# Performance work log

Measured on AMD Instinct MI355X. Metric: run time of the kernel, lower is better.

The kernel has to match this reference:

```python
import jax, jax.numpy as jnp
import numpy as np

# Static config (matches init_kwargs)
N = 1024        # node_num
F = 64          # input_dim (window length)
D = 64          # dim == embed_dim (heads=1)
TOPK = 20
B = 64
EPS = 1e-5      # BatchNorm eps
NEG_SLOPE = 0.2 # GraphLayer leaky_relu slope


def setup_inputs() -> dict:
    key = jax.random.key(0)
    ks = jax.random.split(key, 12)
    s = lambda fan: 1.0 / np.sqrt(fan)
    inp = {
        'data': jax.random.normal(ks[0], (B, N, F), jnp.float32),
        'org_edge_index': jax.random.randint(ks[1], (2, 2048), 0, N),
        'embedding': jax.random.normal(ks[2], (N, D), jnp.float32) * s(D),   # nn.Embedding(node_num, dim), xavier-ish
        'lin_w': jax.random.normal(ks[3], (F, D), jnp.float32) * s(F),       # GraphLayer lin (bias=False)
        'att_i': jax.random.normal(ks[4], (D,), jnp.float32) * s(D),
        'att_j': jax.random.normal(ks[5], (D,), jnp.float32) * s(D),
        'att_em_i': jax.random.normal(ks[6], (D,), jnp.float32) * s(D),
        'att_em_j': jax.random.normal(ks[7], (D,), jnp.float32) * s(D),
        'gnn_bias': jnp.zeros((D,), jnp.float32),
        'bn1_gamma': jnp.ones((D,), jnp.float32),  # GNNLayer.bn
        'bn1_beta': jnp.zeros((D,), jnp.float32),
        'bn2_gamma': jnp.ones((D,), jnp.float32),  # bn_outlayer_in
        'bn2_beta': jnp.zeros((D,), jnp.float32),
        'out_w': jax.random.normal(ks[8], (D, 1), jnp.float32) * s(D),       # OutLayer Linear(dim, 1)
        'out_b': jnp.zeros((1,), jnp.float32),
    }
    return inp


def _batchnorm(x, gamma, beta, axes):
    # training-mode BatchNorm: batch statistics over `axes`, per-feature affine
    mu = jnp.mean(x, axis=axes, keepdims=True)
    var = jnp.var(x, axis=axes, keepdims=True)
    return gamma * (x - mu) * jax.lax.rsqrt(var + EPS) + beta


def reference(data, org_edge_index, embedding, lin_w, att_i, att_j, att_em_i,
              att_em_j, gnn_bias, bn1_gamma, bn1_beta, bn2_gamma, bn2_beta,
              out_w, out_b):
    # --- dynamic graph construction from embedding cosine similarity ---
    w = jax.lax.stop_gradient(embedding)          # weights_arr.detach()
    nrm = jnp.linalg.norm(w, axis=-1)
    cos = (w @ w.T) / jnp.clip(nrm[:, None] * nrm[None, :], 1e-10)
    _, topi = jax.lax.top_k(cos, TOPK)            # [N, TOPK] neighbors j of each target i
    # (torch code drops edges whose cos value is exactly 0 -- measure-zero with
    #  random embeddings; edge count stays N*TOPK. Self edge i->i is always in topk,
    #  matching remove_self_loops + add_self_loops.)

    # --- GraphLayer (GAT-style, heads=1, concat=False, aggr='add') ---
    xl = jnp.einsum('bnf,fd->bnd', data, lin_w)   # linear transform, [B,N,D]
    xj = xl[:, topi]                               # gather neighbor feats [B,N,TOPK,D]
    ej = embedding[topi]                           # neighbor embeddings [N,TOPK,D]
    # alpha = <key_i, att_i||att_em_i> + <key_j, att_j||att_em_j>
    score = (xl @ att_i)[:, :, None] \
          + (embedding @ att_em_i)[None, :, None] \
          + jnp.einsum('bnkd,d->bnk', xj, att_j) \
          + (ej @ att_em_j)[None]                  # [B,N,TOPK]
    alpha = jax.nn.softmax(jax.nn.leaky_relu(score, NEG_SLOPE), axis=-1)
    gnn = jnp.einsum('bnk,bnkd->bnd', alpha, xj) + gnn_bias

    # GNNLayer.bn: BatchNorm1d over B*N samples, D channels
    gnn = _batchnorm(gnn, bn1_gamma, bn1_beta, axes=(0, 1))

    # --- readout ---
    out = gnn * embedding[None]                    # mul with node embedding
    out = jax.nn.relu(_batchnorm(out, bn2_gamma, bn2_beta, axes=(0, 1)))
    # dropout(0.2) -> identity (eval)
    pred = (out @ out_w + out_b).reshape(B, N)     # OutLayer: Linear(D, 1)
    return pred, out
```

## Files before the change

### kernel.cpp

```cpp
#include <hip/hip_runtime.h>

#define NN 1024
#define KK 20
#define BN 65536
#define NEG_SLOPE 0.2f

typedef unsigned short u16;
typedef unsigned int u32;
typedef unsigned long long u64;
typedef __attribute__((ext_vector_type(8))) short bf8;
typedef __attribute__((ext_vector_type(4))) float f32x4;

__device__ __forceinline__ float bf2f(u16 h) {
    return __uint_as_float(((u32)h) << 16);
}
__device__ __forceinline__ u16 f2bf(float f) {
    u32 u = __float_as_uint(f);
    u32 lsb = (u >> 16) & 1u;
    u += 0x7fffu + lsb;
    return (u16)(u >> 16);
}
__device__ __forceinline__ void up2(u32 w, float& a, float& b) {
    a = __uint_as_float(w << 16);
    b = __uint_as_float(w & 0xffff0000u);
}
__device__ __forceinline__ bool is_bf(const void* g1) {
    return *(const u32*)g1 == 0x3F803F80u;
}
template <bool BF>
__device__ __forceinline__ float ldf(const void* p, size_t i) {
    if (BF) return bf2f(((const u16*)p)[i]);
    return ((const float*)p)[i];
}
template <bool BF>
__device__ __forceinline__ void stf(void* p, size_t i, float v) {
    if (BF) ((u16*)p)[i] = f2bf(v);
    else ((float*)p)[i] = v;
}
template <bool BF>
__device__ __forceinline__ void ldf2(const void* p, size_t pairidx, float& a, float& b) {
    if (BF) {
        u32 w = ((const u32*)p)[pairidx];
        up2(w, a, b);
    } else {
        float2 v = ((const float2*)p)[pairidx];
        a = v.x;
        b = v.y;
    }
}

template <bool BF>
__device__ void k1a_body(const void* emb, const void* aei, const void* aej,
                         u16* nwH, u16* nwL, float* e_i, float* e_j, float* stats) {
    __shared__ float sme[4][64], sm2[4][64];
    int tid = threadIdx.x;
    int lane = tid & 63, wave = tid >> 6;
    int n = blockIdx.x * 4 + wave;
    float v = ldf<BF>(emb, n * 64 + lane);
    sme[wave][lane] = v;
    sm2[wave][lane] = v * v;
    float s2 = v * v;
    float si = v * ldf<BF>(aei, lane);
    float sj = v * ldf<BF>(aej, lane);
#pragma unroll
    for (int off = 32; off; off >>= 1) {
        s2 += __shfl_xor(s2, off, 64);
        si += __shfl_xor(si, off, 64);
        sj += __shfl_xor(sj, off, 64);
    }
    float rq = rsqrtf(fmaxf(s2, 1e-20f));
    float x = v * rq;
    u16 h = f2bf(x);
    nwH[n * 64 + lane] = h;
    nwL[n * 64 + lane] = f2bf(x - bf2f(h));
    if (lane == 0) { e_i[n] = si; e_j[n] = sj; }
    __syncthreads();
    if (tid < 64) {
        float u1 = sme[0][tid] + sme[1][tid] + sme[2][tid] + sme[3][tid];
        atomicAdd(&stats[320 + tid], 64.f * u1);
    } else if (tid < 128) {
        int d = tid - 64;
        float u2 = sm2[0][d] + sm2[1][d] + sm2[2][d] + sm2[3][d];
        atomicAdd(&stats[384 + d], 64.f * u2);
    }
}
__global__ __launch_bounds__(256) void k1a_norm(const void* emb, const void* aei, const void* aej,
                                                const void* probe, u16* nwH, u16* nwL,
                                                float* e_i, float* e_j, float* stats) {
    if (is_bf(probe)) k1a_body<true>(emb, aei, aej, nwH, nwL, e_i, e_j, stats);
    else k1a_body<false>(emb, aei, aej, nwH, nwL, e_i, e_j, stats);
}

__global__ __launch_bounds__(256) void k1b_gram(const u16* __restrict__ nwH,
                                                const u16* __restrict__ nwL,
                                                float* __restrict__ G) {
    int tid = threadIdx.x;
    int lane = tid & 63, wave = tid >> 6;
    int c = lane & 15, quad = lane >> 4;
    int rowblk = blockIdx.x >> 4, colblk = blockIdx.x & 15;
    int arow = rowblk * 64 + wave * 16 + c;
    bf8 aH[2], aL[2];
#pragma unroll
    for (int s = 0; s < 2; ++s) {
        aH[s] = *(const bf8*)(nwH + (size_t)arow * 64 + s * 32 + quad * 8);
        aL[s] = *(const bf8*)(nwL + (size_t)arow * 64 + s * 32 + quad * 8);
    }
    f32x4 acc[4] = {{0.f, 0.f, 0.f, 0.f}, {0.f, 0.f, 0.f, 0.f}, {0.f, 0.f, 0.f, 0.f}, {0.f, 0.f, 0.f, 0.f}};
#pragma unroll
    for (int t = 0; t < 4; ++t) {
        int bnode = colblk * 64 + t * 16 + c;
#pragma unroll
        for (int s = 0; s < 2; ++s) {
            bf8 bH = *(const bf8*)(nwH + (size_t)bnode * 64 + s * 32 + quad * 8);
            bf8 bL = *(const bf8*)(nwL + (size_t)bnode * 64 + s * 32 + quad * 8);
            acc[t] = __builtin_amdgcn_mfma_f32_16x16x32_bf16(aH[s], bH, acc[t], 0, 0, 0);
            acc[t] = __builtin_amdgcn_mfma_f32_16x16x32_bf16(aH[s], bL, acc[t], 0, 0, 0);
            acc[t] = __builtin_amdgcn_mfma_f32_16x16x32_bf16(aL[s], bH, acc[t], 0, 0, 0);
        }
    }
#pragma unroll
    for (int t = 0; t < 4; ++t) {
#pragma unroll
        for (int reg = 0; reg < 4; ++reg) {
            int row = rowblk * 64 + wave * 16 + quad * 4 + reg;
            G[(size_t)row * 1024 + colblk * 64 + t * 16 + c] = acc[t][reg];
        }
    }
}

__device__ void k1c_body(int blk, const float* __restrict__ G, int* __restrict__ topi) {
    int lane = threadIdx.x & 63, wave = threadIdx.x >> 6;
    int n = blk * 4 + wave;
    const f32x4* gp = (const f32x4*)(G + (size_t)n * 1024 + lane * 16);
    f32x4 v0 = gp[0], v1 = gp[1], v2 = gp[2], v3 = gp[3];
    float c[16] = {v0.x, v0.y, v0.z, v0.w, v1.x, v1.y, v1.z, v1.w,
                   v2.x, v2.y, v2.z, v2.w, v3.x, v3.y, v3.z, v3.w};
    u32 o[16];
#pragma unroll
    for (int j = 0; j < 16; ++j) {
        u32 u = __float_as_uint(c[j]);
        o[j] = u ^ (u32)(((int)u >> 31) | 0x80000000);
    }
    unsigned mask = 0u;
    int keep = 0;
    for (int r = 0; r < KK; ++r) {
        u32 bo = 0u;
        int bj = 0;
#pragma unroll
        for (int j = 0; j < 16; ++j) {
            bool t = !((mask >> j) & 1u) && o[j] > bo;
            bo = t ? o[j] : bo;
            bj = t ? j : bj;
        }
        u64 key = ((u64)bo << 32) | (u32)(~(u32)(lane * 16 + bj));
#pragma unroll
        for (int off = 32; off; off >>= 1) {
            u64 ok = __shfl_xor((unsigned long long)key, off, 64);
            key = ok > key ? ok : key;
        }
        int bm = (int)((~(u32)key) & 1023u);
        if ((bm >> 4) == lane) mask |= 1u << (bm & 15);
        if (lane == r) keep = bm;
    }
    if (lane < KK) topi[n * KK + lane] = keep;
}

template <bool BF>
__device__ void k2_body(int blk, const void* data, const void* lin_w, const void* att_i,
                        const void* att_j, u16* xl, float* a_i, float* a_j) {
    __shared__ u16 Bl[64 * 72];
    __shared__ u16 Ct[64 * 72];
    int tid = threadIdx.x;
    {
        int k = tid >> 2, n0 = (tid & 3) * 16;
        if (BF) {
            const u16* lw = (const u16*)lin_w;
#pragma unroll
            for (int i = 0; i < 16; ++i) Bl[(n0 + i) * 72 + k] = lw[k * 64 + n0 + i];
        } else {
            const float* lw = (const float*)lin_w;
#pragma unroll
            for (int i = 0; i < 16; ++i) Bl[(n0 + i) * 72 + k] = f2bf(lw[k * 64 + n0 + i]);
        }
    }
    __syncthreads();
    int lane = tid & 63, wave = tid >> 6;
    int c = lane & 15, quad = lane >> 4;
    int m0 = blk * 64 + wave * 16;
    size_t row = (size_t)(m0 + c);
    f32x4 acc[4] = {{0.f, 0.f, 0.f, 0.f}, {0.f, 0.f, 0.f, 0.f}, {0.f, 0.f, 0.f, 0.f}, {0.f, 0.f, 0.f, 0.f}};
#pragma unroll
    for (int s = 0; s < 2; ++s) {
        bf8 a;
        if (BF) {
            a = *(const bf8*)((const u16*)data + row * 64 + s * 32 + quad * 8);
        } else {
            const float* dp = (const float*)data + row * 64 + s * 32 + quad * 8;
            f32x4 x0 = *(const f32x4*)dp;
            f32x4 x1 = *(const f32x4*)(dp + 4);
            a[0] = (short)f2bf(x0.x); a[1] = (short)f2bf(x0.y);
            a[2] = (short)f2bf(x0.z); a[3] = (short)f2bf(x0.w);
            a[4] = (short)f2bf(x1.x); a[5] = (short)f2bf(x1.y);
            a[6] = (short)f2bf(x1.z); a[7] = (short)f2bf(x1.w);
        }
#pragma unroll
        for (int t = 0; t < 4; ++t) {
            bf8 b = *(const bf8*)&Bl[(t * 16 + c) * 72 + s * 32 + quad * 8];
            acc[t] = __builtin_amdgcn_mfma_f32_16x16x32_bf16(a, b, acc[t], 0, 0, 0);
        }
    }
    float wi[4], wj[4];
#pragma unroll
    for (int t = 0; t < 4; ++t) {
        wi[t] = ldf<BF>(att_i, t * 16 + c);
        wj[t] = ldf<BF>(att_j, t * 16 + c);
    }
    float ai4[4] = {0.f, 0.f, 0.f, 0.f}, aj4[4] = {0.f, 0.f, 0.f, 0.f};
#pragma unroll
    for (int t = 0; t < 4; ++t) {
#pragma unroll
        for (int reg = 0; reg < 4; ++reg) {
            float v = acc[t][reg];
            Ct[(wave * 16 + quad * 4 + reg) * 72 + t * 16 + c] = f2bf(v);
            ai4[reg] += v * wi[t];
            aj4[reg] += v * wj[t];
        }
    }
#pragma unroll
    for (int reg = 0; reg < 4; ++reg) {
#pragma unroll
        for (int off = 1; off < 16; off <<= 1) {
            ai4[reg] += __shfl_xor(ai4[reg], off, 64);
            aj4[reg] += __shfl_xor(aj4[reg], off, 64);
        }
    }
    if (c == 0) {
#pragma unroll
        for (int reg = 0; reg < 4; ++reg) {
            a_i[m0 + quad * 4 + reg] = ai4[reg];
            a_j[m0 + quad * 4 + reg] = aj4[reg];
        }
    }
    __syncthreads();
    {
        int r = tid >> 2, seg = tid & 3;
        uint4 v0 = *(const uint4*)&Ct[r * 72 + seg * 16];
        uint4 v1 = *(const uint4*)&Ct[r * 72 + seg * 16 + 8];
        uint4* dst = (uint4*)xl + ((size_t)(blk * 64 + r) * 8 + seg * 2);
        dst[0] = v0;
        dst[1] = v1;
    }
}

__global__ __launch_bounds__(256) void k12_fused(const void* data, const void* lin_w,
                                                 const void* att_i, const void* att_j,
                                                 const void* probe, u16* xl, float* a_i,
                                                 float* a_j, const float* G, int* topi) {
    if (blockIdx.x < 1024) {
        if (is_bf(probe)) k2_body<true>(blockIdx.x, data, lin_w, att_i, att_j, xl, a_i, a_j);
        else k2_body<false>(blockIdx.x, data, lin_w, att_i, att_j, xl, a_i, a_j);
    } else {
        k1c_body(blockIdx.x - 1024, G, topi);
    }
}

template <bool BF>
__device__ void k3_body(const u16* xl, const int* topi, const float* a_i, const float* a_j,
                        const float* e_i, const float* e_j, const void* emb,
                        const void* gnn_bias, void* dout, float* stats) {
    extern __shared__ char smem[];
    u32* slice = (u32*)smem;
    float* aje = (float*)(smem + 131072);
    float* aie = (float*)(smem + 135168);
    uint2* sp = (uint2*)(smem + 136192);
    int tid = threadIdx.x;
    int b = blockIdx.x & 63;
    int q = blockIdx.x >> 6;
    int n0 = q * 256;
    const uint4* src = (const uint4*)(xl + ((size_t)b << 16));
    uint4* dst = (uint4*)slice;
#pragma unroll
    for (int r = 0; r < 8; ++r) dst[r * 1024 + tid] = src[r * 1024 + tid];
    aje[tid] = a_j[(b << 10) + tid] + e_j[tid];
    if (tid < 256) aie[tid] = a_i[(b << 10) + n0 + tid] + e_i[n0 + tid];
    __syncthreads();
    int lane = tid & 63, wave = tid >> 6;
    int half = lane >> 5, hl = lane & 31;
    int hwid = wave * 2 + half;
    float bias0, bias1;
    ldf2<BF>(gnn_bias, hl, bias0, bias1);
    float se[10];
#pragma unroll
    for (int s = 0; s < 10; ++s) se[s] = 0.f;
    int nl0 = hwid * 8;
    u32 tc = 0;
    float al = 0.f;
    {
        int t = (hl < KK) ? topi[(n0 + nl0) * KK + hl] : 0;
        float sc = -3e38f;
        if (hl < KK) {
            sc = aie[nl0] + aje[t];
            sc = sc >= 0.f ? sc : NEG_SLOPE * sc;
        }
        float m = sc;
#pragma unroll
        for (int off = 16; off; off >>= 1) m = fmaxf(m, __shfl_xor(m, off, 32));
        float p = (hl < KK) ? __expf(sc - m) : 0.f;
        float S = p;
#pragma unroll
        for (int off = 16; off; off >>= 1) S += __shfl_xor(S, off, 32);
        tc = (u32)t;
        al = p / S;
    }
    for (int ii = 0; ii < 8; ++ii) {
        int nl = nl0 + ii;
        int n = n0 + nl;
        int pair = (b << 10) + n;
        if (hl < KK) {
            uint2 v; v.x = tc; v.y = __float_as_uint(al);
            sp[hwid * KK + hl] = v;
        }
        u32 tn = 0;
        float aln = 0.f;
        if (ii < 7) {
            int t = (hl < KK) ? topi[(n + 1) * KK + hl] : 0;
            float sc = -3e38f;
            if (hl < KK) {
                sc = aie[nl + 1] + aje[t];
                sc = sc >= 0.f ? sc : NEG_SLOPE * sc;
            }
            float m = sc;
#pragma unroll
            for (int off = 16; off; off >>= 1) m = fmaxf(m, __shfl_xor(m, off, 32));
            float p = (hl < KK) ? __expf(sc - m) : 0.f;
            float S = p;
#pragma unroll
            for (int off = 16; off; off >>= 1) S += __shfl_xor(S, off, 32);
            tn = (u32)t;
            aln = p / S;
        }
        float a0e = 0.f, a0o = 0.f, a1e = 0.f, a1o = 0.f;
#pragma unroll
        for (int k = 0; k < KK; k += 2) {
            uint2 v0 = sp[hwid * KK + k];
            uint2 v1 = sp[hwid * KK + k + 1];
            u32 w0 = slice[(v0.x << 5) + hl];
            u32 w1 = slice[(v1.x << 5) + hl];
            float p0 = __uint_as_float(v0.y);
            float p1 = __uint_as_float(v1.y);
            a0e += p0 * __uint_as_float(w0 << 16);
            a1e += p0 * __uint_as_float(w0 & 0xffff0000u);
            a0o += p1 * __uint_as_float(w1 << 16);
            a1o += p1 * __uint_as_float(w1 & 0xffff0000u);
        }
        float acc0 = a0e + a0o + bias0;
        float acc1 = a1e + a1o + bias1;
        if (BF) {
            u32 pk = (u32)f2bf(acc0) | ((u32)f2bf(acc1) << 16);
            ((u32*)dout)[(BN >> 1) + pair * 32 + hl] = pk;
        } else {
            float2 v2; v2.x = acc0; v2.y = acc1;
            ((float2*)dout)[(BN >> 1) + pair * 32 + hl] = v2;
        }
        float em0, em1;
        ldf2<BF>(emb, n * 32 + hl, em0, em1);
        se[0] += acc0; se[1] += acc1;
        se[2] += acc0 * acc0; se[3] += acc1 * acc1;
        float ge0 = acc0 * em0, ge1 = acc1 * em1;
        se[4] += ge0; se[5] += ge1;
        se[6] += ge0 * ge0; se[7] += ge1 * ge1;
        se[8] += ge0 * em0; se[9] += ge1 * em1;
        tc = tn;
        al = aln;
    }
#pragma unroll
    for (int s = 0; s < 10; ++s) se[s] += __shfl_xor(se[s], 32, 64);
    __syncthreads();
    float* ps = (float*)smem;
    if (half == 0) {
#pragma unroll
        for (int s = 0; s < 5; ++s) {
            ps[wave * 320 + s * 64 + 2 * hl] = se[2 * s];
            ps[wave * 320 + s * 64 + 2 * hl + 1] = se[2 * s + 1];
        }
    }
    __syncthreads();
    if (tid < 320) {
        float s = 0.f;
#pragma unroll
        for (int w = 0; w < 16; ++w) s += ps[w * 320 + tid];
        atomicAdd(&stats[tid], s);
    }
}
__global__ __launch_bounds__(1024) void k3_gnn(const u16* xl, const int* topi, const float* a_i,
                                               const float* a_j, const float* e_i, const float* e_j,
                                               const void* emb, const void* gnn_bias, const void* probe,
                                               void* dout, float* stats) {
    if (is_bf(probe)) k3_body<true>(xl, topi, a_i, a_j, e_i, e_j, emb, gnn_bias, dout, stats);
    else k3_body<false>(xl, topi, a_i, a_j, e_i, e_j, emb, gnn_bias, dout, stats);
}

template <bool BF>
__device__ void k5_body(const void* emb, const float* stats, const void* g1, const void* b1,
                        const void* g2, const void* b2, const void* out_w, const void* out_b,
                        void* dout) {
    int lane = threadIdx.x & 63;
    float P, Q, R;
    {
        int d = lane;
        double inv = 1.0 / 65536.0;
        double S1 = stats[d], S2 = stats[64 + d], T1 = stats[128 + d], T2 = stats[192 + d];
        double T3 = stats[256 + d], U1 = stats[320 + d], U2 = stats[384 + d];
        double mu1 = S1 * inv;
        double var1 = S2 * inv - mu1 * mu1;
        if (var1 < 0.0) var1 = 0.0;
        double r1 = 1.0 / sqrt(var1 + 1e-5);
        double A = (double)ldf<BF>(g1, d) * r1;
        double C = (double)ldf<BF>(b1, d) - A * mu1;
        double E1 = A * T1 + C * U1;
        double mu2 = E1 * inv;
        double E2 = A * A * T2 + 2.0 * A * C * T3 + C * C * U2;
        double var2 = E2 * inv - mu2 * mu2;
        if (var2 < 0.0) var2 = 0.0;
        double r2 = 1.0 / sqrt(var2 + 1e-5);
        double g2r2 = (double)ldf<BF>(g2, d) * r2;
        P = (float)(g2r2 * A);
        Q = (float)(g2r2 * C);
        R = (float)((double)ldf<BF>(b2, d) - g2r2 * mu2);
    }
    int gw = (blockIdx.x * 256 + threadIdx.x) >> 6;
    float wo = ldf<BF>(out_w, lane);
    float ob = ldf<BF>(out_b, 0);
    int row0 = gw * 8;
    for (int i = 0; i < 8; ++i) {
        int row = row0 + i;
        int n = row & 1023;
        size_t oi = (size_t)BN + (size_t)row * 64 + lane;
        float g = ldf<BF>(dout, oi);
        float em = ldf<BF>(emb, n * 64 + lane);
        float o = fmaxf(P * g * em + Q * em + R, 0.f);
        stf<BF>(dout, oi, o);
        float p = o * wo;
#pragma unroll
        for (int off = 32; off; off >>= 1) p += __shfl_xor(p, off, 64);
        if (lane == 0) stf<BF>(dout, row, p + ob);
    }
}
__global__ __launch_bounds__(256) void k5_out(const void* emb, const float* stats, const void* g1,
                                              const void* b1, const void* g2, const void* b2,
                                              const void* out_w, const void* out_b, void* dout) {
    if (is_bf(g1)) k5_body<true>(emb, stats, g1, b1, g2, b2, out_w, out_b, dout);
    else k5_body<false>(emb, stats, g1, b1, g2, b2, out_w, out_b, dout);
}

extern "C" void kernel_launch(void* const* d_in, const int* in_sizes, int n_in,
                              void* d_out, int out_size, void* d_ws, size_t ws_size,
                              hipStream_t stream) {
    const void* data = d_in[0];
    const void* emb = d_in[2];
    const void* lin_w = d_in[3];
    const void* att_i = d_in[4];
    const void* att_j = d_in[5];
    const void* att_em_i = d_in[6];
    const void* att_em_j = d_in[7];
    const void* gnn_bias = d_in[8];
    const void* bn1_g = d_in[9];
    const void* bn1_b = d_in[10];
    const void* bn2_g = d_in[11];
    const void* bn2_b = d_in[12];
    const void* out_w = d_in[13];
    const void* out_b = d_in[14];

    char* ws = (char*)d_ws;
    float* a_i = (float*)ws;
    float* a_j = a_i + 65536;
    float* e_i = a_j + 65536;
    float* e_j = e_i + 1024;
    float* stats = e_j + 1024;
    int* topi = (int*)(stats + 448);
    u16* xl = (u16*)(topi + 20480);
    u16* nwH = xl + 4194304;
    u16* nwL = nwH + 65536;
    float* G = (float*)(nwL + 65536);

    hipMemsetAsync(stats, 0, 448 * sizeof(float), stream);
    k1a_norm<<<256, 256, 0, stream>>>(emb, att_em_i, att_em_j, bn1_g, nwH, nwL, e_i, e_j, stats);
    k1b_gram<<<256, 256, 0, stream>>>(nwH, nwL, G);
    k12_fused<<<1280, 256, 0, stream>>>(data, lin_w, att_i, att_j, bn1_g, xl, a_i, a_j, G, topi);
    k3_gnn<<<256, 1024, 141312, stream>>>(xl, topi, a_i, a_j, e_i, e_j, emb, gnn_bias, bn1_g,
                                          d_out, stats);
    k5_out<<<2048, 256, 0, stream>>>(emb, stats, bn1_g, bn1_b, bn2_g, bn2_b, out_w, out_b, d_out);
}
```

Measured before the change: 161.2 us.

## Precompute softmax weights per node batch and stage GNN output in bf16 scratch

The GNN kernel now computes the attention softmax for all eight nodes of a half-wave up front and stores each neighbor as one packed 32-bit word (bf16 weight plus index) in a larger shared buffer, instead of pipelining one node ahead. The intermediate GNN result is written as bf16 to a dedicated workspace buffer rather than into the output tensor, and the readout kernel reads it from there. This is meant to shorten the dependency chain in the aggregation loop, halve the shared-memory reads for the weights, and cut the intermediate write/read traffic when the output is fp32. The cost is lower precision: both the attention weights and the pre-BN activations are rounded to bf16. Shared memory per block also grows.

```diff
diff --git a/kernel.cpp b/kernel.cpp
--- a/kernel.cpp
+++ b/kernel.cpp
@@ -267,12 +267,12 @@
 template <bool BF>
 __device__ void k3_body(const u16* xl, const int* topi, const float* a_i, const float* a_j,
                         const float* e_i, const float* e_j, const void* emb,
-                        const void* gnn_bias, void* dout, float* stats) {
+                        const void* gnn_bias, u16* gnnb, float* stats) {
     extern __shared__ char smem[];
     u32* slice = (u32*)smem;
     float* aje = (float*)(smem + 131072);
     float* aie = (float*)(smem + 135168);
-    uint2* sp = (uint2*)(smem + 136192);
+    u32* sp = (u32*)(smem + 136192);
     int tid = threadIdx.x;
     int b = blockIdx.x & 63;
     int q = blockIdx.x >> 6;
@@ -287,67 +287,42 @@
     int lane = tid & 63, wave = tid >> 6;
     int half = lane >> 5, hl = lane & 31;
     int hwid = wave * 2 + half;
+    int nl0 = hwid * 8;
+    for (int ii = 0; ii < 8; ++ii) {
+        int nl = nl0 + ii;
+        int t = (hl < KK) ? topi[(n0 + nl) * KK + hl] : 0;
+        float sc = -3e38f;
+        if (hl < KK) {
+            sc = aie[nl] + aje[t];
+            sc = sc >= 0.f ? sc : NEG_SLOPE * sc;
+        }
+        float m = sc;
+#pragma unroll
+        for (int off = 16; off; off >>= 1) m = fmaxf(m, __shfl_xor(m, off, 32));
+        float p = (hl < KK) ? __expf(sc - m) : 0.f;
+        float S = p;
+#pragma unroll
+        for (int off = 16; off; off >>= 1) S += __shfl_xor(S, off, 32);
+        if (hl < KK) sp[(hwid * 8 + ii) * KK + hl] = ((u32)f2bf(p / S) << 16) | (u32)t;
+    }
     float bias0, bias1;
     ldf2<BF>(gnn_bias, hl, bias0, bias1);
     float se[10];
 #pragma unroll
     for (int s = 0; s < 10; ++s) se[s] = 0.f;
-    int nl0 = hwid * 8;
-    u32 tc = 0;
-    float al = 0.f;
-    {
-        int t = (hl < KK) ? topi[(n0 + nl0) * KK + hl] : 0;
-        float sc = -3e38f;
-        if (hl < KK) {
-            sc = aie[nl0] + aje[t];
-            sc = sc >= 0.f ? sc : NEG_SLOPE * sc;
-        }
-        float m = sc;
-#pragma unroll
-        for (int off = 16; off; off >>= 1) m = fmaxf(m, __shfl_xor(m, off, 32));
-        float p = (hl < KK) ? __expf(sc - m) : 0.f;
-        float S = p;
-#pragma unroll
-        for (int off = 16; off; off >>= 1) S += __shfl_xor(S, off, 32);
-        tc = (u32)t;
-        al = p / S;
-    }
     for (int ii = 0; ii < 8; ++ii) {
         int nl = nl0 + ii;
         int n = n0 + nl;
         int pair = (b << 10) + n;
-        if (hl < KK) {
-            uint2 v; v.x = tc; v.y = __float_as_uint(al);
-            sp[hwid * KK + hl] = v;
-        }
-        u32 tn = 0;
-        float aln = 0.f;
-        if (ii < 7) {
-            int t = (hl < KK) ? topi[(n + 1) * KK + hl] : 0;
-            float sc = -3e38f;
-            if (hl < KK) {
-                sc = aie[nl + 1] + aje[t];
-                sc = sc >= 0.f ? sc : NEG_SLOPE * sc;
-            }
-            float m = sc;
-#pragma unroll
-            for (int off = 16; off; off >>= 1) m = fmaxf(m, __shfl_xor(m, off, 32));
-            float p = (hl < KK) ? __expf(sc - m) : 0.f;
-            float S = p;
-#pragma unroll
-            for (int off = 16; off; off >>= 1) S += __shfl_xor(S, off, 32);
-            tn = (u32)t;
-            aln = p / S;
-        }
+        const u32* spp = &sp[(hwid * 8 + ii) * KK];
         float a0e = 0.f, a0o = 0.f, a1e = 0.f, a1o = 0.f;
 #pragma unroll
         for (int k = 0; k < KK; k += 2) {
-            uint2 v0 = sp[hwid * KK + k];
-            uint2 v1 = sp[hwid * KK + k + 1];
-            u32 w0 = slice[(v0.x << 5) + hl];
-            u32 w1 = slice[(v1.x << 5) + hl];
-            float p0 = __uint_as_float(v0.y);
-            float p1 = __uint_as_float(v1.y);
+            uint2 vv = *(const uint2*)&spp[k];
+            u32 w0 = slice[((vv.x & 1023u) << 5) + hl];
+            u32 w1 = slice[((vv.y & 1023u) << 5) + hl];
+            float p0 = __uint_as_float(vv.x & 0xffff0000u);
+            float p1 = __uint_as_float(vv.y & 0xffff0000u);
             a0e += p0 * __uint_as_float(w0 << 16);
             a1e += p0 * __uint_as_float(w0 & 0xffff0000u);
             a0o += p1 * __uint_as_float(w1 << 16);
@@ -355,13 +330,7 @@
         }
         float acc0 = a0e + a0o + bias0;
         float acc1 = a1e + a1o + bias1;
-        if (BF) {
-            u32 pk = (u32)f2bf(acc0) | ((u32)f2bf(acc1) << 16);
-            ((u32*)dout)[(BN >> 1) + pair * 32 + hl] = pk;
-        } else {
-            float2 v2; v2.x = acc0; v2.y = acc1;
-            ((float2*)dout)[(BN >> 1) + pair * 32 + hl] = v2;
-        }
+        ((u32*)gnnb)[pair * 32 + hl] = (u32)f2bf(acc0) | ((u32)f2bf(acc1) << 16);
         float em0, em1;
         ldf2<BF>(emb, n * 32 + hl, em0, em1);
         se[0] += acc0; se[1] += acc1;
@@ -370,8 +339,6 @@
         se[4] += ge0; se[5] += ge1;
         se[6] += ge0 * ge0; se[7] += ge1 * ge1;
         se[8] += ge0 * em0; se[9] += ge1 * em1;
-        tc = tn;
-        al = aln;
     }
 #pragma unroll
     for (int s = 0; s < 10; ++s) se[s] += __shfl_xor(se[s], 32, 64);
@@ -395,15 +362,15 @@
 __global__ __launch_bounds__(1024) void k3_gnn(const u16* xl, const int* topi, const float* a_i,
                                                const float* a_j, const float* e_i, const float* e_j,
                                                const void* emb, const void* gnn_bias, const void* probe,
-                                               void* dout, float* stats) {
-    if (is_bf(probe)) k3_body<true>(xl, topi, a_i, a_j, e_i, e_j, emb, gnn_bias, dout, stats);
-    else k3_body<false>(xl, topi, a_i, a_j, e_i, e_j, emb, gnn_bias, dout, stats);
+                                               u16* gnnb, float* stats) {
+    if (is_bf(probe)) k3_body<true>(xl, topi, a_i, a_j, e_i, e_j, emb, gnn_bias, gnnb, stats);
+    else k3_body<false>(xl, topi, a_i, a_j, e_i, e_j, emb, gnn_bias, gnnb, stats);
 }
 
 template <bool BF>
 __device__ void k5_body(const void* emb, const float* stats, const void* g1, const void* b1,
                         const void* g2, const void* b2, const void* out_w, const void* out_b,
-                        void* dout) {
+                        const u16* gnnb, void* dout) {
     int lane = threadIdx.x & 63;
     float P, Q, R;
     {
@@ -435,11 +402,10 @@
     for (int i = 0; i < 8; ++i) {
         int row = row0 + i;
         int n = row & 1023;
-        size_t oi = (size_t)BN + (size_t)row * 64 + lane;
-        float g = ldf<BF>(dout, oi);
+        float g = bf2f(gnnb[(size_t)row * 64 + lane]);
         float em = ldf<BF>(emb, n * 64 + lane);
         float o = fmaxf(P * g * em + Q * em + R, 0.f);
-        stf<BF>(dout, oi, o);
+        stf<BF>(dout, (size_t)BN + (size_t)row * 64 + lane, o);
         float p = o * wo;
 #pragma unroll
         for (int off = 32; off; off >>= 1) p += __shfl_xor(p, off, 64);
@@ -448,9 +414,10 @@
 }
 __global__ __launch_bounds__(256) void k5_out(const void* emb, const float* stats, const void* g1,
                                               const void* b1, const void* g2, const void* b2,
-                                              const void* out_w, const void* out_b, void* dout) {
-    if (is_bf(g1)) k5_body<true>(emb, stats, g1, b1, g2, b2, out_w, out_b, dout);
-    else k5_body<false>(emb, stats, g1, b1, g2, b2, out_w, out_b, dout);
+                                              const void* out_w, const void* out_b,
+                                              const u16* gnnb, void* dout) {
+    if (is_bf(g1)) k5_body<true>(emb, stats, g1, b1, g2, b2, out_w, out_b, gnnb, dout);
+    else k5_body<false>(emb, stats, g1, b1, g2, b2, out_w, out_b, gnnb, dout);
 }
 
 extern "C" void kernel_launch(void* const* d_in, const int* in_sizes, int n_in,
@@ -482,12 +449,14 @@
     u16* nwH = xl + 4194304;
     u16* nwL = nwH + 65536;
     float* G = (float*)(nwL + 65536);
+    u16* gnnb = (u16*)(G + 1048576);
 
     hipMemsetAsync(stats, 0, 448 * sizeof(float), stream);
     k1a_norm<<<256, 256, 0, stream>>>(emb, att_em_i, att_em_j, bn1_g, nwH, nwL, e_i, e_j, stats);
     k1b_gram<<<256, 256, 0, stream>>>(nwH, nwL, G);
     k12_fused<<<1280, 256, 0, stream>>>(data, lin_w, att_i, att_j, bn1_g, xl, a_i, a_j, G, topi);
-    k3_gnn<<<256, 1024, 141312, stream>>>(xl, topi, a_i, a_j, e_i, e_j, emb, gnn_bias, bn1_g,
-                                          d_out, stats);
-    k5_out<<<2048, 256, 0, stream>>>(emb, stats, bn1_g, bn1_b, bn2_g, bn2_b, out_w, out_b, d_out);
-}
+    k3_gnn<<<256, 1024, 156672, stream>>>(xl, topi, a_i, a_j, e_i, e_j, emb, gnn_bias, bn1_g,
+                                          gnnb, stats);
+    k5_out<<<2048, 256, 0, stream>>>(emb, stats, bn1_g, bn1_b, bn2_g, bn2_b, out_w, out_b,
+                                     gnnb, d_out);
+}
```

Measured after the change: 160.2 us. No clear change (-0.7%).
